# Optimization experiments

Measured on AMD Instinct MI355X. Metric: run time of the kernel, lower is better.

## Reference

```python
import jax, jax.numpy as jnp
import numpy as np

N = 100000      # nodes
E = 600000      # edges
IN, OUT = 128, 32
L1 = IN - (IN - OUT) // 3          # 96
L2 = IN - (2 * (IN - OUT)) // 3    # 64


def setup_inputs() -> dict:
    key = jax.random.key(0)
    ks = jax.random.split(key, 12)

    def lin(k, i, o):
        return jax.random.normal(k, (i, o), jnp.float32) / np.float32(np.sqrt(i))

    return {
        "x": jax.random.normal(ks[0], (N, IN), jnp.float32),
        "edge_index": jax.random.randint(ks[1], (2, E), 0, N, dtype=jnp.int32),
        # ClusterGCNConv 1: lin_out (W,b) + lin_root (no bias)
        "W1": lin(ks[2], IN, L1), "b1": jnp.zeros((L1,), jnp.float32), "Wr1": lin(ks[3], IN, L1),
        # ClusterGCNConv 2
        "W2": lin(ks[4], L1, L2), "b2": jnp.zeros((L2,), jnp.float32), "Wr2": lin(ks[5], L1, L2),
        # GCNConv mu / logstd heads
        "Wmu": lin(ks[6], L2, OUT), "bmu": jnp.zeros((OUT,), jnp.float32),
        "Wls": lin(ks[7], L2, OUT), "bls": jnp.zeros((OUT,), jnp.float32),
    }


def _with_self_loops(edge_index, n):
    loops = jnp.arange(n, dtype=edge_index.dtype)
    src = jnp.concatenate([edge_index[0], loops])
    dst = jnp.concatenate([edge_index[1], loops])
    return src, dst


def _cluster_gcn(x, edge_index, W, b, Wr, n):
    # PyG ClusterGCNConv (diag_lambda=0): out = (D^{-1} (A+I)) x @ W + b + x @ Wr
    src, dst = _with_self_loops(edge_index, n)
    deg = jax.ops.segment_sum(jnp.ones_like(dst, x.dtype), dst, num_segments=n)
    dinv = 1.0 / jnp.clip(deg, 1.0)
    agg = jax.ops.segment_sum(x[src] * dinv[dst][:, None], dst, num_segments=n)
    return agg @ W + b + x @ Wr


def _gcn(x, edge_index, W, b, n):
    # PyG GCNConv: h = x @ W; out = D^{-1/2} (A+I) D^{-1/2} h + b
    h = x @ W
    src, dst = _with_self_loops(edge_index, n)
    deg = jax.ops.segment_sum(jnp.ones_like(dst, h.dtype), dst, num_segments=n)
    dis = jax.lax.rsqrt(jnp.clip(deg, 1.0))  # deg >= 1 thanks to self loops
    norm = dis[src] * dis[dst]
    return jax.ops.segment_sum(h[src] * norm[:, None], dst, num_segments=n) + b


def reference(x, edge_index, W1, b1, Wr1, W2, b2, Wr2, Wmu, bmu, Wls, bls):
    n = x.shape[0]
    h = jax.nn.relu(_cluster_gcn(x, edge_index, W1, b1, Wr1, n))
    h = jax.nn.relu(_cluster_gcn(h, edge_index, W2, b2, Wr2, n))
    return (_gcn(h, edge_index, Wmu, bmu, n), _gcn(h, edge_index, Wls, bls, n))
```

## Files before the change

kernel.cpp:

```cpp
#include <hip/hip_runtime.h>

#define TPB 256

typedef __attribute__((ext_vector_type(8))) short          bf8_t;
typedef __attribute__((ext_vector_type(8))) unsigned short us8_t;
typedef __attribute__((ext_vector_type(4))) float          f4_t;
typedef __attribute__((ext_vector_type(4))) unsigned short us4_t;

__device__ __forceinline__ unsigned short f2bf(float f) {
    union { float f; unsigned u; } v; v.f = f;
    unsigned r = v.u + 0x7FFFu + ((v.u >> 16) & 1u);
    return (unsigned short)(r >> 16);
}
__device__ __forceinline__ float bf2f(unsigned short u) {
    union { unsigned u; float f; } v; v.u = (unsigned)u << 16; return v.f;
}


__global__ void k_count(const int* __restrict__ ei, int E, int* __restrict__ cnt) {
    int e = blockIdx.x * TPB + threadIdx.x;
    if (e < E) atomicAdd(&cnt[ei[E + e]], 1);
}

__global__ void k_blocksum(const int* __restrict__ cnt, int n, int* __restrict__ bsum) {
    __shared__ int s[TPB];
    int t = threadIdx.x, i = blockIdx.x * TPB + t;
    s[t] = (i < n) ? cnt[i] : 0;
    __syncthreads();
    for (int off = TPB / 2; off > 0; off >>= 1) {
        if (t < off) s[t] += s[t + off];
        __syncthreads();
    }
    if (t == 0) bsum[blockIdx.x] = s[0];
}

__global__ void k_scan_bsum(int* __restrict__ bsum, int nb) {
    __shared__ int s[512];
    int t = threadIdx.x;
    int v = (t < nb) ? bsum[t] : 0;
    s[t] = v; __syncthreads();
    for (int off = 1; off < 512; off <<= 1) {
        int x = (t >= off) ? s[t - off] : 0;
        __syncthreads();
        s[t] += x;
        __syncthreads();
    }
    if (t < nb) bsum[t] = s[t] - v;
}

__global__ void k_rowptr(const int* __restrict__ cnt, const int* __restrict__ bsum, int n, int E,
                         int* __restrict__ rowptr, int* __restrict__ cursor,
                         float* __restrict__ dinv, float* __restrict__ dis) {
    __shared__ int s[TPB];
    int t = threadIdx.x, i = blockIdx.x * TPB + t;
    int v = (i < n) ? cnt[i] : 0;
    s[t] = v; __syncthreads();
    for (int off = 1; off < TPB; off <<= 1) {
        int x = (t >= off) ? s[t - off] : 0;
        __syncthreads();
        s[t] += x;
        __syncthreads();
    }
    if (i < n) {
        int start = bsum[blockIdx.x] + s[t] - v;
        rowptr[i] = start;
        cursor[i] = start;
        float d = (float)(v + 1);
        dinv[i] = 1.0f / d;
        dis[i]  = rsqrtf(d);
    }
    if (i == 0) rowptr[n] = E;
}

__global__ void k_fill(const int* __restrict__ ei, int E,
                       int* __restrict__ cursor, int* __restrict__ col) {
    int e = blockIdx.x * TPB + threadIdx.x;
    if (e < E) {
        int src = ei[e], dst = ei[E + e];
        int p = atomicAdd(&cursor[dst], 1);
        col[p] = src;
    }
}

__global__ void k_wconv(const float* W1, const float* Wr1, const float* W2, const float* Wr2,
                        const float* Wmu, const float* Wls,
                        unsigned short* T1, unsigned short* Tr1, unsigned short* T2,
                        unsigned short* Tr2, unsigned short* Tmu, unsigned short* Tls) {
    const float* W; unsigned short* T; int K, M;
    switch (blockIdx.y) {
        case 0: W = W1;  T = T1;  K = 128; M = 96; break;
        case 1: W = Wr1; T = Tr1; K = 128; M = 96; break;
        case 2: W = W2;  T = T2;  K = 96;  M = 64; break;
        case 3: W = Wr2; T = Tr2; K = 96;  M = 64; break;
        case 4: W = Wmu; T = Tmu; K = 64;  M = 32; break;
        default:W = Wls; T = Tls; K = 64;  M = 32; break;
    }
    int idx = blockIdx.x * TPB + threadIdx.x;
    if (idx < K * M) {
        int m = idx / K, k = idx % K;
        T[idx] = f2bf(W[k * M + m]);
    }
}

template <int K, int M, bool AF32>
__global__ __launch_bounds__(TPB) void k_gemm3(const void* __restrict__ Av,
                                               const unsigned short* __restrict__ WT,
                                               unsigned short* __restrict__ Yb,
                                               int n, int nt) {
    constexpr int KS = K / 32;
    constexpr int ST = K + 8;
    __shared__ unsigned short Bs[M * ST];
    for (int i = threadIdx.x * 8; i < M * K; i += TPB * 8) {
        int m = i / K, k = i - m * K;
        *(us8_t*)(Bs + m * ST + k) = *(const us8_t*)(WT + i);
    }
    __syncthreads();

    int lane = threadIdx.x & 63;
    int wave = threadIdx.x >> 6;
    int quad = lane >> 4;
    int l15  = lane & 15;

    for (int tile = blockIdx.x; tile < nt; tile += gridDim.x) {
        int base = tile * 64 + wave * 16;
        int rA = base + l15; if (rA > n - 1) rA = n - 1;

        bf8_t a[KS];
        if (AF32) {
            const float* ap = (const float*)Av + (size_t)rA * K + quad * 8;
#pragma unroll
            for (int s = 0; s < KS; s++) {
                f4_t lo = *(const f4_t*)(ap + s * 32);
                f4_t hi = *(const f4_t*)(ap + s * 32 + 4);
                bf8_t t;
                t[0] = (short)f2bf(lo.x); t[1] = (short)f2bf(lo.y);
                t[2] = (short)f2bf(lo.z); t[3] = (short)f2bf(lo.w);
                t[4] = (short)f2bf(hi.x); t[5] = (short)f2bf(hi.y);
                t[6] = (short)f2bf(hi.z); t[7] = (short)f2bf(hi.w);
                a[s] = t;
            }
        } else {
            const unsigned short* ap = (const unsigned short*)Av + (size_t)rA * K + quad * 8;
#pragma unroll
            for (int s = 0; s < KS; s++) a[s] = *(const bf8_t*)(ap + s * 32);
        }

        int row = base + quad * 4;
#pragma unroll
        for (int ct = 0; ct < M / 16; ct++) {
            const unsigned short* bp = Bs + (ct * 16 + l15) * ST + quad * 8;
            f4_t acc = {0.f, 0.f, 0.f, 0.f};
#pragma unroll
            for (int s = 0; s < KS; s++) {
                bf8_t b = *(const bf8_t*)(bp + s * 32);
                acc = __builtin_amdgcn_mfma_f32_16x16x32_bf16(a[s], b, acc, 0, 0, 0);
            }
            int colg = ct * 16 + l15;
#pragma unroll
            for (int r = 0; r < 4; r++) {
                if (row + r < n) Yb[(size_t)(row + r) * M + colg] = f2bf(acc[r]);
            }
        }
    }
}

__global__ __launch_bounds__(TPB) void k_gemm_out3(const unsigned short* __restrict__ Z,
                                                   const unsigned short* __restrict__ WT,
                                                   const float* __restrict__ bmu,
                                                   const float* __restrict__ bls,
                                                   float* __restrict__ out, int n, int nt) {
    constexpr int K = 64, M = 64, KS = 2, ST = K + 8;
    __shared__ unsigned short Bs[M * ST];
    for (int i = threadIdx.x * 8; i < M * K; i += TPB * 8) {
        int m = i / K, k = i - m * K;
        *(us8_t*)(Bs + m * ST + k) = *(const us8_t*)(WT + i);
    }
    __syncthreads();

    int lane = threadIdx.x & 63;
    int wave = threadIdx.x >> 6;
    int quad = lane >> 4;
    int l15  = lane & 15;

    for (int tile = blockIdx.x; tile < nt; tile += gridDim.x) {
        int base = tile * 64 + wave * 16;
        int rA = base + l15; if (rA > n - 1) rA = n - 1;
        const unsigned short* ap = Z + (size_t)rA * K + quad * 8;
        bf8_t a[KS];
#pragma unroll
        for (int s = 0; s < KS; s++) a[s] = *(const bf8_t*)(ap + s * 32);

        int row = base + quad * 4;
#pragma unroll
        for (int ct = 0; ct < M / 16; ct++) {
            const unsigned short* bp = Bs + (ct * 16 + l15) * ST + quad * 8;
            f4_t acc = {0.f, 0.f, 0.f, 0.f};
#pragma unroll
            for (int s = 0; s < KS; s++) {
                bf8_t b = *(const bf8_t*)(bp + s * 32);
                acc = __builtin_amdgcn_mfma_f32_16x16x32_bf16(a[s], b, acc, 0, 0, 0);
            }
            int colg = ct * 16 + l15;
            float bias = (colg < 32) ? bmu[colg] : bls[colg - 32];
            float* dst = (colg < 32) ? (out + colg) : (out + (size_t)n * 32 + (colg - 32));
#pragma unroll
            for (int r = 0; r < 4; r++) {
                if (row + r < n) dst[(size_t)(row + r) * 32] = acc[r] + bias;
            }
        }
    }
}

template <int MF, int GRP, bool SCALE>
__global__ __launch_bounds__(TPB) void k_aggc(const unsigned short* __restrict__ AB,
                                              const float* __restrict__ bias,
                                              const float* __restrict__ dinv,
                                              const float* __restrict__ dis,
                                              const int* __restrict__ rowptr,
                                              const int* __restrict__ col,
                                              unsigned short* __restrict__ Hb, int n) {
    constexpr int LD = 2 * MF;
    int g = blockIdx.x * (TPB / GRP) + threadIdx.x / GRP;
    int l = threadIdx.x & (GRP - 1);
    if (g >= n) return;
    int c = l * 8;
    if (c >= MF) return;
    int r0 = rowptr[g], r1 = rowptr[g + 1];
    float acc[8];
    {
        bf8_t v = *(const bf8_t*)(AB + (size_t)g * LD + c);
#pragma unroll
        for (int j = 0; j < 8; j++) acc[j] = bf2f((unsigned short)v[j]);
    }
    int e = r0;
    for (; e + 4 <= r1; e += 4) {
        int s0 = col[e], s1 = col[e + 1], s2 = col[e + 2], s3 = col[e + 3];
        bf8_t v0 = *(const bf8_t*)(AB + (size_t)s0 * LD + c);
        bf8_t v1 = *(const bf8_t*)(AB + (size_t)s1 * LD + c);
        bf8_t v2 = *(const bf8_t*)(AB + (size_t)s2 * LD + c);
        bf8_t v3 = *(const bf8_t*)(AB + (size_t)s3 * LD + c);
#pragma unroll
        for (int j = 0; j < 8; j++)
            acc[j] += (bf2f((unsigned short)v0[j]) + bf2f((unsigned short)v1[j]))
                    + (bf2f((unsigned short)v2[j]) + bf2f((unsigned short)v3[j]));
    }
    for (; e < r1; ++e) {
        int s = col[e];
        bf8_t v = *(const bf8_t*)(AB + (size_t)s * LD + c);
#pragma unroll
        for (int j = 0; j < 8; j++) acc[j] += bf2f((unsigned short)v[j]);
    }
    float di = dinv[g];
    float sc = SCALE ? dis[g] : 1.0f;
    bf8_t rr = *(const bf8_t*)(AB + (size_t)g * LD + MF + c);
    us8_t o;
#pragma unroll
    for (int j = 0; j < 8; j++) {
        float h = fmaxf(acc[j] * di + bf2f((unsigned short)rr[j]) + bias[c + j], 0.f);
        o[j] = f2bf(SCALE ? sc * h : h);
    }
    *(us8_t*)(Hb + (size_t)g * MF + c) = o;
}

__global__ __launch_bounds__(TPB) void k_agghead(const unsigned short* __restrict__ H2s,
                                                 const float* __restrict__ dis,
                                                 const int* __restrict__ rowptr,
                                                 const int* __restrict__ col,
                                                 unsigned short* __restrict__ Z, int n) {
    const int GRP = 8;
    int g = blockIdx.x * (TPB / GRP) + threadIdx.x / GRP;
    int l = threadIdx.x & (GRP - 1);
    if (g >= n) return;
    int c = l * 8;
    int r0 = rowptr[g], r1 = rowptr[g + 1];
    float acc[8];
    {
        bf8_t v = *(const bf8_t*)(H2s + (size_t)g * 64 + c);
#pragma unroll
        for (int j = 0; j < 8; j++) acc[j] = bf2f((unsigned short)v[j]);
    }
    int e = r0;
    for (; e + 4 <= r1; e += 4) {
        int s0 = col[e], s1 = col[e + 1], s2 = col[e + 2], s3 = col[e + 3];
        bf8_t v0 = *(const bf8_t*)(H2s + (size_t)s0 * 64 + c);
        bf8_t v1 = *(const bf8_t*)(H2s + (size_t)s1 * 64 + c);
        bf8_t v2 = *(const bf8_t*)(H2s + (size_t)s2 * 64 + c);
        bf8_t v3 = *(const bf8_t*)(H2s + (size_t)s3 * 64 + c);
#pragma unroll
        for (int j = 0; j < 8; j++)
            acc[j] += (bf2f((unsigned short)v0[j]) + bf2f((unsigned short)v1[j]))
                    + (bf2f((unsigned short)v2[j]) + bf2f((unsigned short)v3[j]));
    }
    for (; e < r1; ++e) {
        int s = col[e];
        bf8_t v = *(const bf8_t*)(H2s + (size_t)s * 64 + c);
#pragma unroll
        for (int j = 0; j < 8; j++) acc[j] += bf2f((unsigned short)v[j]);
    }
    float dg = dis[g];
    us8_t o;
#pragma unroll
    for (int j = 0; j < 8; j++) o[j] = f2bf(dg * acc[j]);
    *(us8_t*)(Z + (size_t)g * 64 + c) = o;
}


extern "C" void kernel_launch(void* const* d_in, const int* in_sizes, int n_in,
                              void* d_out, int out_size, void* d_ws, size_t ws_size,
                              hipStream_t stream) {
    const float* x   = (const float*)d_in[0];
    const int*   ei  = (const int*)d_in[1];
    const float* W1  = (const float*)d_in[2];
    const float* b1  = (const float*)d_in[3];
    const float* Wr1 = (const float*)d_in[4];
    const float* W2  = (const float*)d_in[5];
    const float* b2  = (const float*)d_in[6];
    const float* Wr2 = (const float*)d_in[7];
    const float* Wmu = (const float*)d_in[8];
    const float* bmu = (const float*)d_in[9];
    const float* Wls = (const float*)d_in[10];
    const float* bls = (const float*)d_in[11];
    float* out = (float*)d_out;

    const int IN = 128, L1F = 96, L2F = 64;
    const int N = in_sizes[0] / IN;
    const int E = in_sizes[1] / 2;

    char* ws = (char*)d_ws;
    size_t off = 0;
    auto alloc = [&](size_t b) { size_t r = off; off += (b + 255) & ~(size_t)255; return r; };

    const int nb = (N + TPB - 1) / TPB;
    int*   cnt  = (int*)(ws + alloc((size_t)N * 4));
    int*   bsum = (int*)(ws + alloc((size_t)nb * 4));
    int*   rowp = (int*)(ws + alloc((size_t)(N + 1) * 4));
    int*   curs = (int*)(ws + alloc((size_t)N * 4));
    int*   col  = (int*)(ws + alloc((size_t)E * 4));
    float* dinv = (float*)(ws + alloc((size_t)N * 4));
    float* dis  = (float*)(ws + alloc((size_t)N * 4));
    unsigned short* T1  = (unsigned short*)(ws + alloc((size_t)IN  * L1F * 2));
    unsigned short* Tr1 = (unsigned short*)(ws + alloc((size_t)IN  * L1F * 2));
    unsigned short* T2  = (unsigned short*)(ws + alloc((size_t)L1F * L2F * 2));
    unsigned short* Tr2 = (unsigned short*)(ws + alloc((size_t)L1F * L2F * 2));
    unsigned short* Tmu = (unsigned short*)(ws + alloc((size_t)L2F * 32 * 2));
    unsigned short* Tls = (unsigned short*)(ws + alloc((size_t)L2F * 32 * 2));
    unsigned short* AB1 = (unsigned short*)(ws + alloc((size_t)N * 2 * L1F * 2));
    unsigned short* AB2 = (unsigned short*)(ws + alloc((size_t)N * 2 * L2F * 2));
    unsigned short* Hb1 = (unsigned short*)(ws + alloc((size_t)N * L1F * 2));
    unsigned short* H2s = (unsigned short*)(ws + alloc((size_t)N * L2F * 2));
    unsigned short* Zag = (unsigned short*)(ws + alloc((size_t)N * L2F * 2));

    hipMemsetAsync(cnt, 0, (size_t)N * 4, stream);

    dim3 eg((E + TPB - 1) / TPB);
    k_count<<<eg, TPB, 0, stream>>>(ei, E, cnt);
    k_blocksum<<<nb, TPB, 0, stream>>>(cnt, N, bsum);
    k_scan_bsum<<<1, 512, 0, stream>>>(bsum, nb);
    k_rowptr<<<nb, TPB, 0, stream>>>(cnt, bsum, N, E, rowp, curs, dinv, dis);
    k_fill<<<eg, TPB, 0, stream>>>(ei, E, curs, col);

    k_wconv<<<dim3(48, 6), TPB, 0, stream>>>(W1, Wr1, W2, Wr2, Wmu, Wls,
                                             T1, Tr1, T2, Tr2, Tmu, Tls);

    const int nt = (N + 63) / 64;
    k_gemm3<128, 192, true><<<768, TPB, 0, stream>>>(x, T1, AB1, N, nt);
    k_aggc<96, 16, false><<<(N + 15) / 16, TPB, 0, stream>>>(AB1, b1, dinv, dis, rowp, col, Hb1, N);

    k_gemm3<96, 128, false><<<1024, TPB, 0, stream>>>(Hb1, T2, AB2, N, nt);
    k_aggc<64, 8, true><<<(N + 31) / 32, TPB, 0, stream>>>(AB2, b2, dinv, dis, rowp, col, H2s, N);

    k_agghead<<<(N + 31) / 32, TPB, 0, stream>>>(H2s, dis, rowp, col, Zag, N);
    k_gemm_out3<<<1024, TPB, 0, stream>>>(Zag, Tmu, bmu, bls, out, N, nt);
}
```

Before: 288.2 us.

## Hold weight tiles in registers and split GEMM columns across waves

The three dense GEMM kernels no longer stage the transposed bf16 weights in shared memory. Each wave now loads its slice of output columns straight into registers once and keeps it for the whole kernel. Each block works on 16-row tiles, and the four waves share the same A rows while each covers different column tiles. This removes LDS traffic, the shared-memory staging and the __syncthreads, and raises occupancy hints through launch bounds. In exchange, the A rows are loaded redundantly by every wave (cache hits) and the register count grows.

Result: slower. 303.1 us (+5.2%).

```diff
diff --git a/kernel.cpp b/kernel.cpp
--- a/kernel.cpp
+++ b/kernel.cpp
@@ -102,28 +102,29 @@
     }
 }
 
-template <int K, int M, bool AF32>
-__global__ __launch_bounds__(TPB) void k_gemm3(const void* __restrict__ Av,
-                                               const unsigned short* __restrict__ WT,
-                                               unsigned short* __restrict__ Yb,
-                                               int n, int nt) {
+template <int K, int M, int CTW, int MINW, bool AF32>
+__global__ __launch_bounds__(TPB, MINW) void k_gemm8(const void* __restrict__ Av,
+                                                     const unsigned short* __restrict__ WT,
+                                                     unsigned short* __restrict__ Yb,
+                                                     int n, int nt) {
     constexpr int KS = K / 32;
-    constexpr int ST = K + 8;
-    __shared__ unsigned short Bs[M * ST];
-    for (int i = threadIdx.x * 8; i < M * K; i += TPB * 8) {
-        int m = i / K, k = i - m * K;
-        *(us8_t*)(Bs + m * ST + k) = *(const us8_t*)(WT + i);
-    }
-    __syncthreads();
 
     int lane = threadIdx.x & 63;
     int wave = threadIdx.x >> 6;
     int quad = lane >> 4;
     int l15  = lane & 15;
 
-    for (int tile = blockIdx.x; tile < nt; tile += gridDim.x) {
-        int base = tile * 64 + wave * 16;
-        int rA = base + l15; if (rA > n - 1) rA = n - 1;
+    bf8_t breg[CTW][KS];
+#pragma unroll
+    for (int j = 0; j < CTW; j++) {
+        const unsigned short* bp = WT + (size_t)((wave * CTW + j) * 16 + l15) * K + quad * 8;
+#pragma unroll
+        for (int s = 0; s < KS; s++) breg[j][s] = *(const bf8_t*)(bp + s * 32);
+    }
+
+    for (int t = blockIdx.x; t < nt; t += gridDim.x) {
+        int tbase = t * 16;
+        int rA = tbase + l15; if (rA > n - 1) rA = n - 1;
 
         bf8_t a[KS];
         if (AF32) {
@@ -132,12 +133,12 @@
             for (int s = 0; s < KS; s++) {
                 f4_t lo = *(const f4_t*)(ap + s * 32);
                 f4_t hi = *(const f4_t*)(ap + s * 32 + 4);
-                bf8_t t;
-                t[0] = (short)f2bf(lo.x); t[1] = (short)f2bf(lo.y);
-                t[2] = (short)f2bf(lo.z); t[3] = (short)f2bf(lo.w);
-                t[4] = (short)f2bf(hi.x); t[5] = (short)f2bf(hi.y);
-                t[6] = (short)f2bf(hi.z); t[7] = (short)f2bf(hi.w);
-                a[s] = t;
+                bf8_t tv;
+                tv[0] = (short)f2bf(lo.x); tv[1] = (short)f2bf(lo.y);
+                tv[2] = (short)f2bf(lo.z); tv[3] = (short)f2bf(lo.w);
+                tv[4] = (short)f2bf(hi.x); tv[5] = (short)f2bf(hi.y);
+                tv[6] = (short)f2bf(hi.z); tv[7] = (short)f2bf(hi.w);
+                a[s] = tv;
             }
         } else {
             const unsigned short* ap = (const unsigned short*)Av + (size_t)rA * K + quad * 8;
@@ -145,17 +146,14 @@
             for (int s = 0; s < KS; s++) a[s] = *(const bf8_t*)(ap + s * 32);
         }
 
-        int row = base + quad * 4;
-#pragma unroll
-        for (int ct = 0; ct < M / 16; ct++) {
-            const unsigned short* bp = Bs + (ct * 16 + l15) * ST + quad * 8;
+        int row = tbase + quad * 4;
+#pragma unroll
+        for (int j = 0; j < CTW; j++) {
             f4_t acc = {0.f, 0.f, 0.f, 0.f};
 #pragma unroll
-            for (int s = 0; s < KS; s++) {
-                bf8_t b = *(const bf8_t*)(bp + s * 32);
-                acc = __builtin_amdgcn_mfma_f32_16x16x32_bf16(a[s], b, acc, 0, 0, 0);
-            }
-            int colg = ct * 16 + l15;
+            for (int s = 0; s < KS; s++)
+                acc = __builtin_amdgcn_mfma_f32_16x16x32_bf16(a[s], breg[j][s], acc, 0, 0, 0);
+            int colg = (wave * CTW + j) * 16 + l15;
 #pragma unroll
             for (int r = 0; r < 4; r++) {
                 if (row + r < n) Yb[(size_t)(row + r) * M + colg] = f2bf(acc[r]);
@@ -164,49 +162,45 @@
     }
 }
 
-__global__ __launch_bounds__(TPB) void k_gemm_out3(const unsigned short* __restrict__ Z,
-                                                   const unsigned short* __restrict__ WT,
-                                                   const float* __restrict__ bmu,
-                                                   const float* __restrict__ bls,
-                                                   float* __restrict__ out, int n, int nt) {
-    constexpr int K = 64, M = 64, KS = 2, ST = K + 8;
-    __shared__ unsigned short Bs[M * ST];
-    for (int i = threadIdx.x * 8; i < M * K; i += TPB * 8) {
-        int m = i / K, k = i - m * K;
-        *(us8_t*)(Bs + m * ST + k) = *(const us8_t*)(WT + i);
-    }
-    __syncthreads();
+__global__ __launch_bounds__(TPB, 8) void k_gemm_out8(const unsigned short* __restrict__ Z,
+                                                      const unsigned short* __restrict__ WT,
+                                                      const float* __restrict__ bmu,
+                                                      const float* __restrict__ bls,
+                                                      float* __restrict__ out, int n, int nt) {
+    constexpr int K = 64, KS = 2;
 
     int lane = threadIdx.x & 63;
     int wave = threadIdx.x >> 6;
     int quad = lane >> 4;
     int l15  = lane & 15;
 
-    for (int tile = blockIdx.x; tile < nt; tile += gridDim.x) {
-        int base = tile * 64 + wave * 16;
-        int rA = base + l15; if (rA > n - 1) rA = n - 1;
+    bf8_t breg[KS];
+    {
+        const unsigned short* bp = WT + (size_t)(wave * 16 + l15) * K + quad * 8;
+#pragma unroll
+        for (int s = 0; s < KS; s++) breg[s] = *(const bf8_t*)(bp + s * 32);
+    }
+    int colg = wave * 16 + l15;
+    float bias = (colg < 32) ? bmu[colg] : bls[colg - 32];
+    float* dstc = (colg < 32) ? (out + colg) : (out + (size_t)n * 32 + (colg - 32));
+
+    for (int t = blockIdx.x; t < nt; t += gridDim.x) {
+        int tbase = t * 16;
+        int rA = tbase + l15; if (rA > n - 1) rA = n - 1;
         const unsigned short* ap = Z + (size_t)rA * K + quad * 8;
         bf8_t a[KS];
 #pragma unroll
         for (int s = 0; s < KS; s++) a[s] = *(const bf8_t*)(ap + s * 32);
 
-        int row = base + quad * 4;
-#pragma unroll
-        for (int ct = 0; ct < M / 16; ct++) {
-            const unsigned short* bp = Bs + (ct * 16 + l15) * ST + quad * 8;
-            f4_t acc = {0.f, 0.f, 0.f, 0.f};
-#pragma unroll
-            for (int s = 0; s < KS; s++) {
-                bf8_t b = *(const bf8_t*)(bp + s * 32);
-                acc = __builtin_amdgcn_mfma_f32_16x16x32_bf16(a[s], b, acc, 0, 0, 0);
-            }
-            int colg = ct * 16 + l15;
-            float bias = (colg < 32) ? bmu[colg] : bls[colg - 32];
-            float* dst = (colg < 32) ? (out + colg) : (out + (size_t)n * 32 + (colg - 32));
-#pragma unroll
-            for (int r = 0; r < 4; r++) {
-                if (row + r < n) dst[(size_t)(row + r) * 32] = acc[r] + bias;
-            }
+        f4_t acc = {0.f, 0.f, 0.f, 0.f};
+#pragma unroll
+        for (int s = 0; s < KS; s++)
+            acc = __builtin_amdgcn_mfma_f32_16x16x32_bf16(a[s], breg[s], acc, 0, 0, 0);
+
+        int row = tbase + quad * 4;
+#pragma unroll
+        for (int r = 0; r < 4; r++) {
+            if (row + r < n) dstc[(size_t)(row + r) * 32] = acc[r] + bias;
         }
     }
 }
@@ -362,13 +356,14 @@
     k_wconv<<<dim3(48, 6), TPB, 0, stream>>>(W1, Wr1, W2, Wr2, Wmu, Wls,
                                              T1, Tr1, T2, Tr2, Tmu, Tls);
 
-    const int nt = (N + 63) / 64;
-    k_gemm3<128, 192, true><<<768, TPB, 0, stream>>>(x, T1, AB1, N, nt);
+    const int nt = (N + 15) / 16;
+    const int gg = 2048;
+    k_gemm8<128, 192, 3, 4, true><<<gg, TPB, 0, stream>>>(x, T1, AB1, N, nt);
     k_aggc<96, 16, false><<<(N + 15) / 16, TPB, 0, stream>>>(AB1, b1, dinv, dis, rowp, col, Hb1, N);
 
-    k_gemm3<96, 128, false><<<1024, TPB, 0, stream>>>(Hb1, T2, AB2, N, nt);
+    k_gemm8<96, 128, 2, 6, false><<<gg, TPB, 0, stream>>>(Hb1, T2, AB2, N, nt);
     k_aggc<64, 8, true><<<(N + 31) / 32, TPB, 0, stream>>>(AB2, b2, dinv, dis, rowp, col, H2s, N);
 
     k_agghead<<<(N + 31) / 32, TPB, 0, stream>>>(H2s, dis, rowp, col, Zag, N);
-    k_gemm_out3<<<1024, TPB, 0, stream>>>(Zag, Tmu, bmu, bls, out, N, nt);
-}
+    k_gemm_out8<<<gg, TPB, 0, stream>>>(Zag, Tmu, bmu, bls, out, N, nt);
+}
```

## Fuse layer-1 aggregation into layer-2 GEMM and head aggregation into output GEMM

Applied to the files above, without the earlier changes.

Two kernel pairs are merged into persistent kernels. In each, a block gathers neighbor rows for a small node tile into double-buffered shared memory, then runs MFMA against weights held in registers. This removes the Hb1 and Zag intermediate buffers and their global write and read round trips, plus two launches. In exchange, each tile has a barrier between gather and GEMM, tiles are small (16 and 32 rows), and in k_fuse1 a quarter of the threads sit idle during the gather phase.

New measurement: 281.4 us, median of 2. 1.02x faster.

```diff
diff --git a/kernel.cpp b/kernel.cpp
--- a/kernel.cpp
+++ b/kernel.cpp
@@ -164,48 +164,87 @@
     }
 }
 
-__global__ __launch_bounds__(TPB) void k_gemm_out3(const unsigned short* __restrict__ Z,
-                                                   const unsigned short* __restrict__ WT,
-                                                   const float* __restrict__ bmu,
-                                                   const float* __restrict__ bls,
-                                                   float* __restrict__ out, int n, int nt) {
-    constexpr int K = 64, M = 64, KS = 2, ST = K + 8;
-    __shared__ unsigned short Bs[M * ST];
-    for (int i = threadIdx.x * 8; i < M * K; i += TPB * 8) {
-        int m = i / K, k = i - m * K;
-        *(us8_t*)(Bs + m * ST + k) = *(const us8_t*)(WT + i);
-    }
-    __syncthreads();
-
-    int lane = threadIdx.x & 63;
-    int wave = threadIdx.x >> 6;
-    int quad = lane >> 4;
-    int l15  = lane & 15;
-
-    for (int tile = blockIdx.x; tile < nt; tile += gridDim.x) {
-        int base = tile * 64 + wave * 16;
-        int rA = base + l15; if (rA > n - 1) rA = n - 1;
-        const unsigned short* ap = Z + (size_t)rA * K + quad * 8;
-        bf8_t a[KS];
-#pragma unroll
-        for (int s = 0; s < KS; s++) a[s] = *(const bf8_t*)(ap + s * 32);
-
-        int row = base + quad * 4;
-#pragma unroll
-        for (int ct = 0; ct < M / 16; ct++) {
-            const unsigned short* bp = Bs + (ct * 16 + l15) * ST + quad * 8;
-            f4_t acc = {0.f, 0.f, 0.f, 0.f};
+__global__ __launch_bounds__(TPB, 4) void k_fuse1(const unsigned short* __restrict__ AB,
+                                                  const unsigned short* __restrict__ WT2,
+                                                  const float* __restrict__ bias,
+                                                  const float* __restrict__ dinv,
+                                                  const int* __restrict__ rowptr,
+                                                  const int* __restrict__ col,
+                                                  unsigned short* __restrict__ AB2,
+                                                  int n, int nt) {
+    constexpr int LDA = 192, MF = 96, ST1 = 104, KS = 3, M2 = 128;
+    __shared__ unsigned short Hs[2][16 * ST1];
+
+    int t = threadIdx.x;
+    int lane = t & 63, wave = t >> 6, quad = lane >> 4, l15 = lane & 15;
+
+    bf8_t breg[2][KS];
+#pragma unroll
+    for (int j = 0; j < 2; j++) {
+        const unsigned short* bp = WT2 + (size_t)((wave * 2 + j) * 16 + l15) * 96 + quad * 8;
+#pragma unroll
+        for (int s = 0; s < KS; s++) breg[j][s] = *(const bf8_t*)(bp + s * 32);
+    }
+
+    int gl = t >> 4;
+    int cg = t & 15;
+    int c  = cg * 8;
+    bool p1act = (c < MF);
+
+    int p = 0;
+    for (int tile = blockIdx.x; tile < nt; tile += gridDim.x, p ^= 1) {
+        int tbase = tile * 16;
+        if (p1act) {
+            int g = tbase + gl; if (g > n - 1) g = n - 1;
+            int r0 = rowptr[g], r1 = rowptr[g + 1];
+            float acc[8];
+            {
+                bf8_t v = *(const bf8_t*)(AB + (size_t)g * LDA + c);
+#pragma unroll
+                for (int j = 0; j < 8; j++) acc[j] = bf2f((unsigned short)v[j]);
+            }
+            int e = r0;
+            for (; e + 4 <= r1; e += 4) {
+                int s0 = col[e], s1 = col[e + 1], s2 = col[e + 2], s3 = col[e + 3];
+                bf8_t v0 = *(const bf8_t*)(AB + (size_t)s0 * LDA + c);
+                bf8_t v1 = *(const bf8_t*)(AB + (size_t)s1 * LDA + c);
+                bf8_t v2 = *(const bf8_t*)(AB + (size_t)s2 * LDA + c);
+                bf8_t v3 = *(const bf8_t*)(AB + (size_t)s3 * LDA + c);
+#pragma unroll
+                for (int j = 0; j < 8; j++)
+                    acc[j] += (bf2f((unsigned short)v0[j]) + bf2f((unsigned short)v1[j]))
+                            + (bf2f((unsigned short)v2[j]) + bf2f((unsigned short)v3[j]));
+            }
+            for (; e < r1; ++e) {
+                int s = col[e];
+                bf8_t v = *(const bf8_t*)(AB + (size_t)s * LDA + c);
+#pragma unroll
+                for (int j = 0; j < 8; j++) acc[j] += bf2f((unsigned short)v[j]);
+            }
+            float di = dinv[g];
+            bf8_t rr = *(const bf8_t*)(AB + (size_t)g * LDA + MF + c);
+            us8_t o;
+#pragma unroll
+            for (int j = 0; j < 8; j++)
+                o[j] = f2bf(fmaxf(acc[j] * di + bf2f((unsigned short)rr[j]) + bias[c + j], 0.f));
+            *(us8_t*)(&Hs[p][gl * ST1 + c]) = o;
+        }
+        __syncthreads();
+
+        int row = tbase + quad * 4;
+#pragma unroll
+        for (int j = 0; j < 2; j++) {
+            const unsigned short* apl = &Hs[p][l15 * ST1 + quad * 8];
+            f4_t acc2 = {0.f, 0.f, 0.f, 0.f};
 #pragma unroll
             for (int s = 0; s < KS; s++) {
-                bf8_t b = *(const bf8_t*)(bp + s * 32);
-                acc = __builtin_amdgcn_mfma_f32_16x16x32_bf16(a[s], b, acc, 0, 0, 0);
-            }
-            int colg = ct * 16 + l15;
-            float bias = (colg < 32) ? bmu[colg] : bls[colg - 32];
-            float* dst = (colg < 32) ? (out + colg) : (out + (size_t)n * 32 + (colg - 32));
+                bf8_t a = *(const bf8_t*)(apl + s * 32);
+                acc2 = __builtin_amdgcn_mfma_f32_16x16x32_bf16(a, breg[j][s], acc2, 0, 0, 0);
+            }
+            int colg = (wave * 2 + j) * 16 + l15;
 #pragma unroll
             for (int r = 0; r < 4; r++) {
-                if (row + r < n) dst[(size_t)(row + r) * 32] = acc[r] + bias;
+                if (row + r < n) AB2[(size_t)(row + r) * M2 + colg] = f2bf(acc2[r]);
             }
         }
     }
@@ -262,46 +301,88 @@
     *(us8_t*)(Hb + (size_t)g * MF + c) = o;
 }
 
-__global__ __launch_bounds__(TPB) void k_agghead(const unsigned short* __restrict__ H2s,
-                                                 const float* __restrict__ dis,
-                                                 const int* __restrict__ rowptr,
-                                                 const int* __restrict__ col,
-                                                 unsigned short* __restrict__ Z, int n) {
-    const int GRP = 8;
-    int g = blockIdx.x * (TPB / GRP) + threadIdx.x / GRP;
-    int l = threadIdx.x & (GRP - 1);
-    if (g >= n) return;
-    int c = l * 8;
-    int r0 = rowptr[g], r1 = rowptr[g + 1];
-    float acc[8];
+__global__ __launch_bounds__(TPB, 4) void k_fuse2(const unsigned short* __restrict__ H2s,
+                                                  const unsigned short* __restrict__ WTo,
+                                                  const float* __restrict__ bmu,
+                                                  const float* __restrict__ bls,
+                                                  const float* __restrict__ dis,
+                                                  const int* __restrict__ rowptr,
+                                                  const int* __restrict__ col,
+                                                  float* __restrict__ out, int n, int nt) {
+    constexpr int ST2 = 72, KS = 2;
+    __shared__ unsigned short Zs[2][32 * ST2];
+
+    int t = threadIdx.x;
+    int lane = t & 63, wave = t >> 6, quad = lane >> 4, l15 = lane & 15;
+
+    bf8_t breg[KS];
     {
-        bf8_t v = *(const bf8_t*)(H2s + (size_t)g * 64 + c);
-#pragma unroll
-        for (int j = 0; j < 8; j++) acc[j] = bf2f((unsigned short)v[j]);
-    }
-    int e = r0;
-    for (; e + 4 <= r1; e += 4) {
-        int s0 = col[e], s1 = col[e + 1], s2 = col[e + 2], s3 = col[e + 3];
-        bf8_t v0 = *(const bf8_t*)(H2s + (size_t)s0 * 64 + c);
-        bf8_t v1 = *(const bf8_t*)(H2s + (size_t)s1 * 64 + c);
-        bf8_t v2 = *(const bf8_t*)(H2s + (size_t)s2 * 64 + c);
-        bf8_t v3 = *(const bf8_t*)(H2s + (size_t)s3 * 64 + c);
-#pragma unroll
-        for (int j = 0; j < 8; j++)
-            acc[j] += (bf2f((unsigned short)v0[j]) + bf2f((unsigned short)v1[j]))
-                    + (bf2f((unsigned short)v2[j]) + bf2f((unsigned short)v3[j]));
-    }
-    for (; e < r1; ++e) {
-        int s = col[e];
-        bf8_t v = *(const bf8_t*)(H2s + (size_t)s * 64 + c);
-#pragma unroll
-        for (int j = 0; j < 8; j++) acc[j] += bf2f((unsigned short)v[j]);
-    }
-    float dg = dis[g];
-    us8_t o;
-#pragma unroll
-    for (int j = 0; j < 8; j++) o[j] = f2bf(dg * acc[j]);
-    *(us8_t*)(Z + (size_t)g * 64 + c) = o;
+        const unsigned short* bp = WTo + (size_t)(wave * 16 + l15) * 64 + quad * 8;
+#pragma unroll
+        for (int s = 0; s < KS; s++) breg[s] = *(const bf8_t*)(bp + s * 32);
+    }
+    int colg = wave * 16 + l15;
+    float bias = (colg < 32) ? bmu[colg] : bls[colg - 32];
+    float* dstc = (colg < 32) ? (out + colg) : (out + (size_t)n * 32 + (colg - 32));
+
+    int gl = t >> 3;
+    int c  = (t & 7) * 8;
+
+    int p = 0;
+    for (int tile = blockIdx.x; tile < nt; tile += gridDim.x, p ^= 1) {
+        int tbase = tile * 32;
+        {
+            int g = tbase + gl; if (g > n - 1) g = n - 1;
+            int r0 = rowptr[g], r1 = rowptr[g + 1];
+            float acc[8];
+            {
+                bf8_t v = *(const bf8_t*)(H2s + (size_t)g * 64 + c);
+#pragma unroll
+                for (int j = 0; j < 8; j++) acc[j] = bf2f((unsigned short)v[j]);
+            }
+            int e = r0;
+            for (; e + 4 <= r1; e += 4) {
+                int s0 = col[e], s1 = col[e + 1], s2 = col[e + 2], s3 = col[e + 3];
+                bf8_t v0 = *(const bf8_t*)(H2s + (size_t)s0 * 64 + c);
+                bf8_t v1 = *(const bf8_t*)(H2s + (size_t)s1 * 64 + c);
+                bf8_t v2 = *(const bf8_t*)(H2s + (size_t)s2 * 64 + c);
+                bf8_t v3 = *(const bf8_t*)(H2s + (size_t)s3 * 64 + c);
+#pragma unroll
+                for (int j = 0; j < 8; j++)
+                    acc[j] += (bf2f((unsigned short)v0[j]) + bf2f((unsigned short)v1[j]))
+                            + (bf2f((unsigned short)v2[j]) + bf2f((unsigned short)v3[j]));
+            }
+            for (; e < r1; ++e) {
+                int s = col[e];
+                bf8_t v = *(const bf8_t*)(H2s + (size_t)s * 64 + c);
+#pragma unroll
+                for (int j = 0; j < 8; j++) acc[j] += bf2f((unsigned short)v[j]);
+            }
+            float dg = dis[g];
+            us8_t o;
+#pragma unroll
+            for (int j = 0; j < 8; j++) o[j] = f2bf(dg * acc[j]);
+            *(us8_t*)(&Zs[p][gl * ST2 + c]) = o;
+        }
+        __syncthreads();
+
+#pragma unroll
+        for (int st = 0; st < 2; st++) {
+            const unsigned short* apl = &Zs[p][(st * 16 + l15) * ST2 + quad * 8];
+            bf8_t a[KS];
+#pragma unroll
+            for (int s = 0; s < KS; s++) a[s] = *(const bf8_t*)(apl + s * 32);
+            f4_t acc = {0.f, 0.f, 0.f, 0.f};
+#pragma unroll
+            for (int s = 0; s < KS; s++)
+                acc = __builtin_amdgcn_mfma_f32_16x16x32_bf16(a[s], breg[s], acc, 0, 0, 0);
+            int row = tbase + st * 16 + quad * 4;
+#pragma unroll
+            for (int r = 0; r < 4; r++) {
+                if (row + r < n) dstc[(size_t)(row + r) * 32] = acc[r] + bias;
+            }
+        }
+    }
 }
 
 
@@ -346,9 +427,8 @@
     unsigned short* Tls = (unsigned short*)(ws + alloc((size_t)L2F * 32 * 2));
     unsigned short* AB1 = (unsigned short*)(ws + alloc((size_t)N * 2 * L1F * 2));
     unsigned short* AB2 = (unsigned short*)(ws + alloc((size_t)N * 2 * L2F * 2));
-    unsigned short* Hb1 = (unsigned short*)(ws + alloc((size_t)N * L1F * 2));
     unsigned short* H2s = (unsigned short*)(ws + alloc((size_t)N * L2F * 2));
-    unsigned short* Zag = (unsigned short*)(ws + alloc((size_t)N * L2F * 2));
+    (void)Tr1; (void)Tr2; (void)Tls;
 
     hipMemsetAsync(cnt, 0, (size_t)N * 4, stream);
 
@@ -362,13 +442,14 @@
     k_wconv<<<dim3(48, 6), TPB, 0, stream>>>(W1, Wr1, W2, Wr2, Wmu, Wls,
                                              T1, Tr1, T2, Tr2, Tmu, Tls);
 
-    const int nt = (N + 63) / 64;
-    k_gemm3<128, 192, true><<<768, TPB, 0, stream>>>(x, T1, AB1, N, nt);
-    k_aggc<96, 16, false><<<(N + 15) / 16, TPB, 0, stream>>>(AB1, b1, dinv, dis, rowp, col, Hb1, N);
-
-    k_gemm3<96, 128, false><<<1024, TPB, 0, stream>>>(Hb1, T2, AB2, N, nt);
+    const int nt64 = (N + 63) / 64;
+    k_gemm3<128, 192, true><<<768, TPB, 0, stream>>>(x, T1, AB1, N, nt64);
+
+    const int nt16 = (N + 15) / 16;
+    k_fuse1<<<2048, TPB, 0, stream>>>(AB1, T2, b1, dinv, rowp, col, AB2, N, nt16);
+
     k_aggc<64, 8, true><<<(N + 31) / 32, TPB, 0, stream>>>(AB2, b2, dinv, dis, rowp, col, H2s, N);
 
-    k_agghead<<<(N + 31) / 32, TPB, 0, stream>>>(H2s, dis, rowp, col, Zag, N);
-    k_gemm_out3<<<1024, TPB, 0, stream>>>(Zag, Tmu, bmu, bls, out, N, nt);
-}
+    const int nt32 = (N + 31) / 32;
+    k_fuse2<<<2048, TPB, 0, stream>>>(H2s, Tmu, bmu, bls, dis, rowp, col, out, N, nt32);
+}
```
